# Performance work log

Hardware: AMD Instinct MI355X
Metric: run time of the kernel (lower is better)

The kernel has to match this reference:

```python
import jax, jax.numpy as jnp
import numpy as np

B, ENC, DEC, H, OUT = 4096, 168, 24, 64, 1
IN = 1 + 5 + 3 + 4 + 7  # 20


def _lstm_step(xt, h, c, Wih, Whh, bih, bhh):
    # PyTorch gate order: i, f, g, o
    g = xt @ Wih.T + h @ Whh.T + bih + bhh
    i, f, gg, o = jnp.split(g, 4, axis=-1)
    c = jax.nn.sigmoid(f) * c + jax.nn.sigmoid(i) * jnp.tanh(gg)
    h = jax.nn.sigmoid(o) * jnp.tanh(c)
    return h, c


def _lstm_layer(x, Wih, Whh, bih, bhh):
    # x: [T, B, in] -> ys: [T, B, H], final (h, c)
    h0 = jnp.zeros((x.shape[1], Whh.shape[1]), x.dtype)

    def step(carry, xt):
        h, c = _lstm_step(xt, carry[0], carry[1], Wih, Whh, bih, bhh)
        return (h, c), h

    (h, c), ys = jax.lax.scan(step, (h0, h0), x)
    return ys, h, c


def setup_inputs() -> dict:
    key = jax.random.key(0)
    ks = jax.random.split(key, 24)
    rn = lambda k, s, sc=0.05: jax.random.normal(k, s, jnp.float32) * sc
    inp = {
        "input_p_q": rn(ks[0], (B, ENC, 1), 1.0),
        "input_time": jax.random.randint(ks[1], (B, ENC, 4), 0, 8),
        "label_p": rn(ks[2], (B, ENC), 1.0),
        "decoder_time": jax.random.randint(ks[3], (B, DEC, 4), 0, 8),
        # encoder LSTM layer 0
        "enc0_Wih": rn(ks[4], (4 * H, IN)), "enc0_Whh": rn(ks[5], (4 * H, H)),
        "enc0_bih": rn(ks[6], (4 * H,)), "enc0_bhh": rn(ks[7], (4 * H,)),
        # encoder LSTM layer 1
        "enc1_Wih": rn(ks[8], (4 * H, H)), "enc1_Whh": rn(ks[9], (4 * H, H)),
        "enc1_bih": rn(ks[10], (4 * H,)), "enc1_bhh": rn(ks[11], (4 * H,)),
        # decoder LSTMCell (input = OUT + 19 = 20)
        "dec_Wih": rn(ks[12], (4 * H, OUT + 19)), "dec_Whh": rn(ks[13], (4 * H, H)),
        "dec_bih": rn(ks[14], (4 * H,)), "dec_bhh": rn(ks[15], (4 * H,)),
        # output projection
        "Wout": rn(ks[16], (OUT, H)), "bout": rn(ks[17], (OUT,)),
        # embeddings
        "emb_hour": rn(ks[18], (24, 5)), "emb_wd": rn(ks[19], (8, 3)),
        "emb_mo": rn(ks[20], (13, 4)), "emb_woy": rn(ks[21], (54, 7)),
    }
    return inp


def reference(input_p_q, input_time, label_p, decoder_time,
              enc0_Wih, enc0_Whh, enc0_bih, enc0_bhh,
              enc1_Wih, enc1_Whh, enc1_bih, enc1_bhh,
              dec_Wih, dec_Whh, dec_bih, dec_bhh,
              Wout, bout, emb_hour, emb_wd, emb_mo, emb_woy):
    def time_feats(t):  # t: [B, T, 4] int -> [B, T, 19]
        return jnp.concatenate([emb_hour[t[:, :, 0]], emb_wd[t[:, :, 1]],
                                emb_mo[t[:, :, 2]], emb_woy[t[:, :, 3]]], axis=-1)

    input_q = label_p[:, :ENC, None]                      # [B, ENC, 1]
    enc_in = jnp.concatenate([input_q, time_feats(input_time)], axis=-1)  # [B, ENC, 20]
    x = enc_in.transpose(1, 0, 2)                         # [ENC, B, 20]
    ys0, _, _ = _lstm_layer(x, enc0_Wih, enc0_Whh, enc0_bih, enc0_bhh)
    _, h1, c1 = _lstm_layer(ys0, enc1_Wih, enc1_Whh, enc1_bih, enc1_bhh)

    dec_feat = time_feats(decoder_time).transpose(1, 0, 2)  # [DEC, B, 19]
    prev0 = label_p[:, ENC - 1, None]                       # [B, 1]

    def dec_step(carry, ft):
        h, c, prev = carry
        xin = jnp.concatenate([prev, ft], axis=-1)          # [B, 20]
        h, c = _lstm_step(xin, h, c, dec_Wih, dec_Whh, dec_bih, dec_bhh)
        out = h @ Wout.T + bout                             # [B, OUT]
        return (h, c, out), out

    _, outs = jax.lax.scan(dec_step, (h1, c1, prev0), dec_feat)
    return outs.transpose(1, 0, 2)                          # [B, DEC, OUT]
```

## Files before the change

### kernel.cpp

```cpp
#include <hip/hip_runtime.h>

#define DEVFN __device__ __forceinline__

typedef float  f32x4  __attribute__((ext_vector_type(4)));
typedef short  bf16x8 __attribute__((ext_vector_type(8)));

constexpr int ENC = 168;
constexpr int DEC = 24;
constexpr int BT  = 16;
constexpr int NBLK = 4096 / BT;

constexpr float LOG2E  = 1.4426950408889634f;
constexpr float LOG2E2 = 2.8853900817779268f;

constexpr int W0F = 0;
constexpr int W1F = 24576;
constexpr int WDF = 57344;
constexpr int F_B0   = 40960;
constexpr int F_B1   = 41216;
constexpr int F_BD   = 41472;
constexpr int F_WOUT = 41728;
constexpr int F_BOUT = 41792;
constexpr int F_EMB  = 41793;
constexpr int NEMB = 574;

DEVFN ushort f2bf(float v) {
    unsigned b = __float_as_uint(v);
    return (ushort)((b + 0x7FFFu + ((b >> 16) & 1u)) >> 16);
}
DEVFN float bf2f(ushort u) { return __uint_as_float(((unsigned)u) << 16); }
DEVFN unsigned cvt_pk_bf16(float a, float b) {
    unsigned r;
    asm("v_cvt_pk_bf16_f32 %0, %1, %2" : "=v"(r) : "v"(a), "v"(b));
    return r;
}
DEVFN float exp2n(float x) {
    float r;
    asm("v_exp_f32 %0, -%1" : "=v"(r) : "v"(x));
    return r;
}
DEVFN void pinv(bf16x8& v) { asm volatile("" : "+v"(v)); }
DEVFN void pinf(f32x4& v)  { asm volatile("" : "+v"(v)); }

DEVFN float lstm_cell(float gi, float gf, float gg, float go, float& c) {
    float a  = exp2n(fmaxf(gi, -21.f));
    float b  = exp2n(fmaxf(gg, -43.f));
    float f  = exp2n(gf);
    float sf = __builtin_amdgcn_rcpf(1.f + f);
    float it = (1.f - b) * __builtin_amdgcn_rcpf(fmaf(a, b, a + b + 1.f));
    c = fmaf(sf, c, it);
    float d  = exp2n(fmaxf(c, -15.f) * LOG2E2);
    float o  = exp2n(fmaxf(go, -21.f));
    return (1.f - d) * __builtin_amdgcn_rcpf(fmaf(o, d, o + d + 1.f));
}

__global__ void prep_kernel(
    const float* __restrict__ w0ih, const float* __restrict__ w0hh,
    const float* __restrict__ b0ih, const float* __restrict__ b0hh,
    const float* __restrict__ w1ih, const float* __restrict__ w1hh,
    const float* __restrict__ b1ih, const float* __restrict__ b1hh,
    const float* __restrict__ wdih, const float* __restrict__ wdhh,
    const float* __restrict__ bdih, const float* __restrict__ bdhh,
    const float* __restrict__ wout, const float* __restrict__ boutp,
    const float* __restrict__ eh,   const float* __restrict__ ewd,
    const float* __restrict__ emo,  const float* __restrict__ ewoy,
    void* __restrict__ ws)
{
    ushort* wsu = (ushort*)ws;
    float*  wsf = (float*)ws;
    const int total = 81920 + 1407;
    for (int idx = blockIdx.x * blockDim.x + threadIdx.x; idx < total;
         idx += gridDim.x * blockDim.x) {
        if (idx < 81920) {
            int layer, q;
            if (idx < W1F)      { layer = 0; q = idx; }
            else if (idx < WDF) { layer = 1; q = idx - W1F; }
            else                { layer = 2; q = idx - WDF; }
            int c  = q >> 13;
            int tt = (q >> 9) & 15;
            int l  = (q >> 3) & 63;
            int j  = q & 7;
            int k  = c * 32 + (l >> 4) * 8 + j;
            int n  = tt * 16 + (l & 15);
            float v = 0.f;
            if (layer == 0) {
                if (k < 20) v = w0ih[n * 20 + k];
                else if (k == 20) v = w0ih[n * 20];
                else if (k >= 32 && k < 96) v = w0hh[n * 64 + (k - 32)];
            } else if (layer == 1) {
                if (k < 64) v = w1ih[n * 64 + k];
                else        v = w1hh[n * 64 + (k - 64)];
            } else {
                if (k < 20) v = wdih[n * 20 + k];
                else if (k == 20) v = wdih[n * 20];
                else if (k >= 32 && k < 96) v = wdhh[n * 64 + (k - 32)];
            }
            v *= ((n >> 6) == 2) ? LOG2E2 : LOG2E;
            wsu[idx] = f2bf(v);
        } else {
            int f = idx - 81920;
            float v;
            if (f < 768) {
                float sc = (((f & 255) >> 6) == 2) ? LOG2E2 : LOG2E;
                if (f < 256)      v = (b0ih[f] + b0hh[f]) * sc;
                else if (f < 512) v = (b1ih[f - 256] + b1hh[f - 256]) * sc;
                else              v = (bdih[f - 512] + bdhh[f - 512]) * sc;
            }
            else if (f < 832) v = wout[f - 768];
            else if (f == 832) v = boutp[0];
            else {
                int e = f - 833;
                if (e < 120)      v = eh[e];
                else if (e < 144) v = ewd[e - 120];
                else if (e < 196) v = emo[e - 144];
                else              v = ewoy[e - 196];
            }
            wsf[40960 + f] = v;
        }
    }
}

DEVFN int offX(int k, int m) {
    return (m + 16 * (k >> 3)) * 8 + (k & 7);
}
DEVFN void store_h4(ushort* A, int off, const float* h) {
    unsigned h01 = cvt_pk_bf16(h[0], h[1]);
    unsigned h23 = cvt_pk_bf16(h[2], h[3]);
    asm volatile("" : "+v"(h01), "+v"(h23));
    unsigned long long p = ((unsigned long long)h23 << 32) | h01;
    *(unsigned long long*)(A + off) = p;
}
DEVFN void store_prev(ushort* A, int m, float v) {
    ushort hi = f2bf(v);
    A[offX(0, m)]  = hi;
    A[offX(20, m)] = f2bf(v - bf2f(hi));
}

__global__ __launch_bounds__(512)
__attribute__((amdgpu_waves_per_eu(2, 2)))
void lstm_mfma(
    const int* __restrict__ input_time, const float* __restrict__ label_p,
    const int* __restrict__ decoder_time, const void* __restrict__ ws,
    float* __restrict__ out)
{
    const ushort* wsu = (const ushort*)ws;
    const float*  wsf = (const float*)ws;

    __shared__ __align__(16) ushort Abuf[2][5 * 512];
    __shared__ float s_emb[NEMB];
    __shared__ float s_wout[64];
    __shared__ float sh1[16 * 68];
    __shared__ float s_bout;

    const int tid = threadIdx.x;
    const int w   = tid >> 6;
    const int l   = tid & 63;
    const int q   = l >> 4;
    const int m   = l & 15;
    const int wl  = w & 3;
    const bool isL0 = (w < 4);
    const int b0g = blockIdx.x * BT;
    const int u0  = wl * 16 + q * 4;

    const int hoff = (1 + (u0 >> 5)) * 512 +
                     (m + 16 * ((u0 & 31) >> 3)) * 8 + (u0 & 7) +
                     (isL0 ? 0 : 1024);

    for (int i = tid; i < 2 * 5 * 512; i += 512) ((ushort*)Abuf)[i] = 0;
    for (int i = tid; i < NEMB; i += 512) s_emb[i] = wsf[F_EMB + i];
    if (tid < 64) s_wout[tid] = wsf[F_WOUT + tid];
    if (tid == 0) s_bout = wsf[F_BOUT];

    bf16x8 wA[4][4];
    if (isL0) {
#pragma unroll
        for (int c = 0; c < 3; c++)
#pragma unroll
            for (int g = 0; g < 4; g++)
                wA[c][g] = *(const bf16x8*)(wsu + W0F +
                    (c * 16 + g * 4 + wl) * 512 + l * 8);
        wA[3][0] = wA[3][1] = wA[3][2] = wA[3][3] = bf16x8{0,0,0,0,0,0,0,0};
    } else {
#pragma unroll
        for (int c = 0; c < 4; c++)
#pragma unroll
            for (int g = 0; g < 4; g++)
                wA[c][g] = *(const bf16x8*)(wsu + W1F +
                    (c * 16 + g * 4 + wl) * 512 + l * 8);
    }
#pragma unroll
    for (int c = 0; c < 4; c++)
#pragma unroll
        for (int g = 0; g < 4; g++) pinv(wA[c][g]);

    f32x4 biasv[4];
#pragma unroll
    for (int g = 0; g < 4; g++) {
        biasv[g] = *(const f32x4*)(wsf + (isL0 ? F_B0 : F_B1) + g * 64 + u0);
        pinf(biasv[g]);
    }

    float cst[4] = {0.f, 0.f, 0.f, 0.f};

    const int kk1 = tid >> 4;
    const int kk2 = kk1 + 16;
    const bool bx2 = (tid < 64);
    int sel1 = 0, estr1 = 0, ebase1 = 0;
    if (kk1 >= 1) {
        int f = kk1 - 1;
        if (f < 5)       { sel1 = 0; estr1 = 5; ebase1 = 0   + f; }
        else if (f < 8)  { sel1 = 1; estr1 = 3; ebase1 = 120 + (f - 5); }
        else if (f < 12) { sel1 = 2; estr1 = 4; ebase1 = 144 + (f - 8); }
        else             { sel1 = 3; estr1 = 7; ebase1 = 196 + (f - 12); }
    }
    const int ebase2 = 196 + (kk2 - 13);

    __syncthreads();
    if (isL0) {
        if (kk1 == 0) {
            store_prev(Abuf[0], m, label_p[(b0g + m) * ENC]);
        } else {
            int idx = input_time[((b0g + m) * ENC) * 4 + sel1];
            Abuf[0][offX(kk1, m)] = f2bf(s_emb[ebase1 + idx * estr1]);
        }
        if (bx2) {
            int idx2 = input_time[((b0g + m) * ENC) * 4 + 3];
            Abuf[0][offX(kk2, m)] = f2bf(s_emb[ebase2 + idx2 * 7]);
        }
    }
    __syncthreads();

    for (int i = 0; i <= ENC; ++i) {
        const ushort* Ar = Abuf[i & 1];
        ushort* Aw = Abuf[(i + 1) & 1];
        const bool active = isL0 ? (i < ENC) : (i >= 1);

        float pre_f = 0.f; int pre_i1 = 0, pre_i2 = 0;
        const bool encX  = (i + 1 < ENC) && isL0;
        const bool decX0 = (i == ENC) && isL0;
        if (encX) {
            if (kk1 == 0) pre_f  = label_p[(b0g + m) * ENC + (i + 1)];
            else          pre_i1 = input_time[((b0g + m) * ENC + (i + 1)) * 4 + sel1];
            if (bx2)      pre_i2 = input_time[((b0g + m) * ENC + (i + 1)) * 4 + 3];
        } else if (decX0) {
            if (kk1 == 0) pre_f  = label_p[(b0g + m) * ENC + (ENC - 1)];
            else          pre_i1 = decoder_time[((b0g + m) * DEC) * 4 + sel1];
            if (bx2)      pre_i2 = decoder_time[((b0g + m) * DEC) * 4 + 3];
        }

        if (active) {
            f32x4 acc[4];
            if (isL0) {
                bf16x8 ah[3];
#pragma unroll
                for (int c = 0; c < 3; c++)
                    ah[c] = *(const bf16x8*)(Ar + c * 512 + l * 8);
#pragma unroll
                for (int g = 0; g < 4; g++)
                    acc[g] = __builtin_amdgcn_mfma_f32_16x16x32_bf16(
                        wA[0][g], ah[0], biasv[g], 0, 0, 0);
#pragma unroll
                for (int c = 1; c < 3; c++)
#pragma unroll
                    for (int g = 0; g < 4; g++)
                        acc[g] = __builtin_amdgcn_mfma_f32_16x16x32_bf16(
                            wA[c][g], ah[c], acc[g], 0, 0, 0);
            } else {
                bf16x8 ah[4];
#pragma unroll
                for (int c = 0; c < 4; c++)
                    ah[c] = *(const bf16x8*)(Ar + (1 + c) * 512 + l * 8);
#pragma unroll
                for (int g = 0; g < 4; g++)
                    acc[g] = __builtin_amdgcn_mfma_f32_16x16x32_bf16(
                        wA[0][g], ah[0], biasv[g], 0, 0, 0);
#pragma unroll
                for (int c = 1; c < 4; c++)
#pragma unroll
                    for (int g = 0; g < 4; g++)
                        acc[g] = __builtin_amdgcn_mfma_f32_16x16x32_bf16(
                            wA[c][g], ah[c], acc[g], 0, 0, 0);
            }
            float hv[4];
#pragma unroll
            for (int r = 0; r < 4; r++)
                hv[r] = lstm_cell(acc[0][r], acc[1][r], acc[2][r], acc[3][r], cst[r]);
            store_h4(Aw, hoff, hv);
        }
        if (encX || decX0) {
            if (kk1 == 0) store_prev(Aw, m, pre_f);
            else          Aw[offX(kk1, m)] = f2bf(s_emb[ebase1 + pre_i1 * estr1]);
            if (bx2)      Aw[offX(kk2, m)] = f2bf(s_emb[ebase2 + pre_i2 * 7]);
        }
        __syncthreads();
    }

    if (!isL0) {
#pragma unroll
        for (int c = 0; c < 3; c++)
#pragma unroll
            for (int g = 0; g < 4; g++)
                wA[c][g] = *(const bf16x8*)(wsu + WDF +
                    (c * 16 + g * 4 + wl) * 512 + l * 8);
#pragma unroll
        for (int c = 0; c < 3; c++)
#pragma unroll
            for (int g = 0; g < 4; g++) pinv(wA[c][g]);
#pragma unroll
        for (int g = 0; g < 4; g++) {
            biasv[g] = *(const f32x4*)(wsf + F_BD + g * 64 + u0);
            pinf(biasv[g]);
        }
    }

    for (int t = 0; t < DEC; ++t) {
        const ushort* Ar = Abuf[(t + 1) & 1];
        ushort* Aw = Abuf[t & 1];

        int pre_i1 = 0, pre_i2 = 0;
        const bool dX = (t + 1 < DEC) && isL0;
        if (dX) {
            if (kk1 >= 1) pre_i1 = decoder_time[((b0g + m) * DEC + (t + 1)) * 4 + sel1];
            if (bx2)      pre_i2 = decoder_time[((b0g + m) * DEC + (t + 1)) * 4 + 3];
        }

        if (!isL0) {
            bf16x8 ah[3];
            ah[0] = *(const bf16x8*)(Ar + 0 * 512 + l * 8);
            ah[1] = *(const bf16x8*)(Ar + 3 * 512 + l * 8);
            ah[2] = *(const bf16x8*)(Ar + 4 * 512 + l * 8);
            f32x4 acc[4];
#pragma unroll
            for (int g = 0; g < 4; g++)
                acc[g] = __builtin_amdgcn_mfma_f32_16x16x32_bf16(
                    wA[0][g], ah[0], biasv[g], 0, 0, 0);
#pragma unroll
            for (int c = 1; c < 3; c++)
#pragma unroll
                for (int g = 0; g < 4; g++)
                    acc[g] = __builtin_amdgcn_mfma_f32_16x16x32_bf16(
                        wA[c][g], ah[c], acc[g], 0, 0, 0);
            float hv[4];
#pragma unroll
            for (int r = 0; r < 4; r++)
                hv[r] = lstm_cell(acc[0][r], acc[1][r], acc[2][r], acc[3][r], cst[r]);
            store_h4(Aw, hoff, hv);
            *(f32x4*)&sh1[m * 68 + u0] = *(f32x4*)hv;
        }
        if (dX && kk1 >= 1) Aw[offX(kk1, m)] = f2bf(s_emb[ebase1 + pre_i1 * estr1]);
        if (dX && bx2)      Aw[offX(kk2, m)] = f2bf(s_emb[ebase2 + pre_i2 * 7]);
        __syncthreads();

        if (tid < 16) {
            float a = s_bout;
#pragma unroll 16
            for (int u = 0; u < 64; u++) a = fmaf(s_wout[u], sh1[tid * 68 + u], a);
            out[(b0g + tid) * DEC + t] = a;
            if (t + 1 < DEC) store_prev(Aw, tid, a);
        }
        __syncthreads();
    }
}

extern "C" void kernel_launch(void* const* d_in, const int* in_sizes, int n_in,
                              void* d_out, int out_size, void* d_ws, size_t ws_size,
                              hipStream_t stream)
{
    typedef const float* fp;
    const int* input_time   = (const int*)d_in[1];
    fp         label_p      = (fp)d_in[2];
    const int* decoder_time = (const int*)d_in[3];

    prep_kernel<<<128, 256, 0, stream>>>(
        (fp)d_in[4],  (fp)d_in[5],  (fp)d_in[6],  (fp)d_in[7],
        (fp)d_in[8],  (fp)d_in[9],  (fp)d_in[10], (fp)d_in[11],
        (fp)d_in[12], (fp)d_in[13], (fp)d_in[14], (fp)d_in[15],
        (fp)d_in[16], (fp)d_in[17],
        (fp)d_in[18], (fp)d_in[19], (fp)d_in[20], (fp)d_in[21],
        d_ws);

    lstm_mfma<<<NBLK, 512, 0, stream>>>(
        input_time, label_p, decoder_time, d_ws, (float*)d_out);
}
```

Before: 285.2 us.

## Merge both encoder layers into each wave with 256-thread blocks

Each block drops from 8 waves (4 for layer 0, 4 for layer 1) to 4 waves, and every wave now computes both the layer-0 and the layer-1 gate MFMAs plus both cell updates for its hidden-unit slice. Both layers' weights are kept in registers, and waves_per_eu is set to 1. The goal is to cut the per-step barrier cost and wave imbalance by doubling the independent MFMA work per wave, which gives more ILP within a step. The cost is higher register pressure, fewer resident waves per CU, and twice the serial work per wave on each timestep.

Result: slower. 360.8 us (+26.5%).

```diff
diff --git a/kernel.cpp b/kernel.cpp
--- a/kernel.cpp
+++ b/kernel.cpp
@@ -136,8 +136,8 @@
     A[offX(20, m)] = f2bf(v - bf2f(hi));
 }
 
-__global__ __launch_bounds__(512)
-__attribute__((amdgpu_waves_per_eu(2, 2)))
+__global__ __launch_bounds__(256)
+__attribute__((amdgpu_waves_per_eu(1, 1)))
 void lstm_mfma(
     const int* __restrict__ input_time, const float* __restrict__ label_p,
     const int* __restrict__ decoder_time, const void* __restrict__ ws,
@@ -157,50 +157,45 @@
     const int l   = tid & 63;
     const int q   = l >> 4;
     const int m   = l & 15;
-    const int wl  = w & 3;
-    const bool isL0 = (w < 4);
     const int b0g = blockIdx.x * BT;
-    const int u0  = wl * 16 + q * 4;
-
-    const int hoff = (1 + (u0 >> 5)) * 512 +
-                     (m + 16 * ((u0 & 31) >> 3)) * 8 + (u0 & 7) +
-                     (isL0 ? 0 : 1024);
-
-    for (int i = tid; i < 2 * 5 * 512; i += 512) ((ushort*)Abuf)[i] = 0;
-    for (int i = tid; i < NEMB; i += 512) s_emb[i] = wsf[F_EMB + i];
+    const int u0  = w * 16 + q * 4;
+
+    const int hoff0 = (1 + (u0 >> 5)) * 512 +
+                      (m + 16 * ((u0 & 31) >> 3)) * 8 + (u0 & 7);
+    const int hoff1 = hoff0 + 1024;
+
+    for (int i = tid; i < 2 * 5 * 512; i += 256) ((ushort*)Abuf)[i] = 0;
+    for (int i = tid; i < NEMB; i += 256) s_emb[i] = wsf[F_EMB + i];
     if (tid < 64) s_wout[tid] = wsf[F_WOUT + tid];
     if (tid == 0) s_bout = wsf[F_BOUT];
 
-    bf16x8 wA[4][4];
-    if (isL0) {
-#pragma unroll
-        for (int c = 0; c < 3; c++)
-#pragma unroll
-            for (int g = 0; g < 4; g++)
-                wA[c][g] = *(const bf16x8*)(wsu + W0F +
-                    (c * 16 + g * 4 + wl) * 512 + l * 8);
-        wA[3][0] = wA[3][1] = wA[3][2] = wA[3][3] = bf16x8{0,0,0,0,0,0,0,0};
-    } else {
-#pragma unroll
-        for (int c = 0; c < 4; c++)
-#pragma unroll
-            for (int g = 0; g < 4; g++)
-                wA[c][g] = *(const bf16x8*)(wsu + W1F +
-                    (c * 16 + g * 4 + wl) * 512 + l * 8);
-    }
+    bf16x8 wA0[3][4], wA1[4][4];
+#pragma unroll
+    for (int c = 0; c < 3; c++)
+#pragma unroll
+        for (int g = 0; g < 4; g++) {
+            wA0[c][g] = *(const bf16x8*)(wsu + W0F +
+                (c * 16 + g * 4 + w) * 512 + l * 8);
+            pinv(wA0[c][g]);
+        }
 #pragma unroll
     for (int c = 0; c < 4; c++)
 #pragma unroll
-        for (int g = 0; g < 4; g++) pinv(wA[c][g]);
-
-    f32x4 biasv[4];
+        for (int g = 0; g < 4; g++) {
+            wA1[c][g] = *(const bf16x8*)(wsu + W1F +
+                (c * 16 + g * 4 + w) * 512 + l * 8);
+            pinv(wA1[c][g]);
+        }
+    f32x4 bias0[4], bias1[4];
 #pragma unroll
     for (int g = 0; g < 4; g++) {
-        biasv[g] = *(const f32x4*)(wsf + (isL0 ? F_B0 : F_B1) + g * 64 + u0);
-        pinf(biasv[g]);
-    }
-
-    float cst[4] = {0.f, 0.f, 0.f, 0.f};
+        bias0[g] = *(const f32x4*)(wsf + F_B0 + g * 64 + u0);
+        bias1[g] = *(const f32x4*)(wsf + F_B1 + g * 64 + u0);
+        pinf(bias0[g]); pinf(bias1[g]);
+    }
+
+    float cst0[4] = {0.f, 0.f, 0.f, 0.f};
+    float cst1[4] = {0.f, 0.f, 0.f, 0.f};
 
     const int kk1 = tid >> 4;
     const int kk2 = kk1 + 16;
@@ -216,7 +211,7 @@
     const int ebase2 = 196 + (kk2 - 13);
 
     __syncthreads();
-    if (isL0) {
+    {
         if (kk1 == 0) {
             store_prev(Abuf[0], m, label_p[(b0g + m) * ENC]);
         } else {
@@ -233,11 +228,11 @@
     for (int i = 0; i <= ENC; ++i) {
         const ushort* Ar = Abuf[i & 1];
         ushort* Aw = Abuf[(i + 1) & 1];
-        const bool active = isL0 ? (i < ENC) : (i >= 1);
+        const bool L0 = (i < ENC), L1 = (i >= 1);
 
         float pre_f = 0.f; int pre_i1 = 0, pre_i2 = 0;
-        const bool encX  = (i + 1 < ENC) && isL0;
-        const bool decX0 = (i == ENC) && isL0;
+        const bool encX  = (i + 1 < ENC);
+        const bool decX0 = (i == ENC);
         if (encX) {
             if (kk1 == 0) pre_f  = label_p[(b0g + m) * ENC + (i + 1)];
             else          pre_i1 = input_time[((b0g + m) * ENC + (i + 1)) * 4 + sel1];
@@ -248,44 +243,49 @@
             if (bx2)      pre_i2 = decoder_time[((b0g + m) * DEC) * 4 + 3];
         }
 
-        if (active) {
-            f32x4 acc[4];
-            if (isL0) {
-                bf16x8 ah[3];
-#pragma unroll
-                for (int c = 0; c < 3; c++)
-                    ah[c] = *(const bf16x8*)(Ar + c * 512 + l * 8);
+        bf16x8 a[5];
+#pragma unroll
+        for (int c = 0; c < 5; c++)
+            a[c] = *(const bf16x8*)(Ar + c * 512 + l * 8);
+
+        f32x4 acc0[4], acc1[4];
+        if (L0) {
+#pragma unroll
+            for (int g = 0; g < 4; g++)
+                acc0[g] = __builtin_amdgcn_mfma_f32_16x16x32_bf16(
+                    wA0[0][g], a[0], bias0[g], 0, 0, 0);
+#pragma unroll
+            for (int c = 1; c < 3; c++)
 #pragma unroll
                 for (int g = 0; g < 4; g++)
-                    acc[g] = __builtin_amdgcn_mfma_f32_16x16x32_bf16(
-                        wA[0][g], ah[0], biasv[g], 0, 0, 0);
-#pragma unroll
-                for (int c = 1; c < 3; c++)
-#pragma unroll
-                    for (int g = 0; g < 4; g++)
-                        acc[g] = __builtin_amdgcn_mfma_f32_16x16x32_bf16(
-                            wA[c][g], ah[c], acc[g], 0, 0, 0);
-            } else {
-                bf16x8 ah[4];
-#pragma unroll
-                for (int c = 0; c < 4; c++)
-                    ah[c] = *(const bf16x8*)(Ar + (1 + c) * 512 + l * 8);
+                    acc0[g] = __builtin_amdgcn_mfma_f32_16x16x32_bf16(
+                        wA0[c][g], a[c], acc0[g], 0, 0, 0);
+        }
+        if (L1) {
+#pragma unroll
+            for (int g = 0; g < 4; g++)
+                acc1[g] = __builtin_amdgcn_mfma_f32_16x16x32_bf16(
+                    wA1[0][g], a[1], bias1[g], 0, 0, 0);
+#pragma unroll
+            for (int c = 1; c < 4; c++)
 #pragma unroll
                 for (int g = 0; g < 4; g++)
-                    acc[g] = __builtin_amdgcn_mfma_f32_16x16x32_bf16(
-                        wA[0][g], ah[0], biasv[g], 0, 0, 0);
-#pragma unroll
-                for (int c = 1; c < 4; c++)
-#pragma unroll
-                    for (int g = 0; g < 4; g++)
-                        acc[g] = __builtin_amdgcn_mfma_f32_16x16x32_bf16(
-                            wA[c][g], ah[c], acc[g], 0, 0, 0);
-            }
+                    acc1[g] = __builtin_amdgcn_mfma_f32_16x16x32_bf16(
+                        wA1[c][g], a[1 + c], acc1[g], 0, 0, 0);
+        }
+        if (L0) {
             float hv[4];
 #pragma unroll
             for (int r = 0; r < 4; r++)
-                hv[r] = lstm_cell(acc[0][r], acc[1][r], acc[2][r], acc[3][r], cst[r]);
-            store_h4(Aw, hoff, hv);
+                hv[r] = lstm_cell(acc0[0][r], acc0[1][r], acc0[2][r], acc0[3][r], cst0[r]);
+            store_h4(Aw, hoff0, hv);
+        }
+        if (L1) {
+            float hv[4];
+#pragma unroll
+            for (int r = 0; r < 4; r++)
+                hv[r] = lstm_cell(acc1[0][r], acc1[1][r], acc1[2][r], acc1[3][r], cst1[r]);
+            store_h4(Aw, hoff1, hv);
         }
         if (encX || decX0) {
             if (kk1 == 0) store_prev(Aw, m, pre_f);
@@ -295,22 +295,18 @@
         __syncthreads();
     }
 
-    if (!isL0) {
-#pragma unroll
-        for (int c = 0; c < 3; c++)
-#pragma unroll
-            for (int g = 0; g < 4; g++)
-                wA[c][g] = *(const bf16x8*)(wsu + WDF +
-                    (c * 16 + g * 4 + wl) * 512 + l * 8);
-#pragma unroll
-        for (int c = 0; c < 3; c++)
-#pragma unroll
-            for (int g = 0; g < 4; g++) pinv(wA[c][g]);
+#pragma unroll
+    for (int c = 0; c < 3; c++)
 #pragma unroll
         for (int g = 0; g < 4; g++) {
-            biasv[g] = *(const f32x4*)(wsf + F_BD + g * 64 + u0);
-            pinf(biasv[g]);
-        }
+            wA0[c][g] = *(const bf16x8*)(wsu + WDF +
+                (c * 16 + g * 4 + w) * 512 + l * 8);
+            pinv(wA0[c][g]);
+        }
+#pragma unroll
+    for (int g = 0; g < 4; g++) {
+        bias0[g] = *(const f32x4*)(wsf + F_BD + g * 64 + u0);
+        pinf(bias0[g]);
     }
 
     for (int t = 0; t < DEC; ++t) {
@@ -318,13 +314,13 @@
         ushort* Aw = Abuf[t & 1];
 
         int pre_i1 = 0, pre_i2 = 0;
-        const bool dX = (t + 1 < DEC) && isL0;
+        const bool dX = (t + 1 < DEC);
         if (dX) {
             if (kk1 >= 1) pre_i1 = decoder_time[((b0g + m) * DEC + (t + 1)) * 4 + sel1];
             if (bx2)      pre_i2 = decoder_time[((b0g + m) * DEC + (t + 1)) * 4 + 3];
         }
 
-        if (!isL0) {
+        {
             bf16x8 ah[3];
             ah[0] = *(const bf16x8*)(Ar + 0 * 512 + l * 8);
             ah[1] = *(const bf16x8*)(Ar + 3 * 512 + l * 8);
@@ -333,18 +329,18 @@
 #pragma unroll
             for (int g = 0; g < 4; g++)
                 acc[g] = __builtin_amdgcn_mfma_f32_16x16x32_bf16(
-                    wA[0][g], ah[0], biasv[g], 0, 0, 0);
+                    wA0[0][g], ah[0], bias0[g], 0, 0, 0);
 #pragma unroll
             for (int c = 1; c < 3; c++)
 #pragma unroll
                 for (int g = 0; g < 4; g++)
                     acc[g] = __builtin_amdgcn_mfma_f32_16x16x32_bf16(
-                        wA[c][g], ah[c], acc[g], 0, 0, 0);
+                        wA0[c][g], ah[c], acc[g], 0, 0, 0);
             float hv[4];
 #pragma unroll
             for (int r = 0; r < 4; r++)
-                hv[r] = lstm_cell(acc[0][r], acc[1][r], acc[2][r], acc[3][r], cst[r]);
-            store_h4(Aw, hoff, hv);
+                hv[r] = lstm_cell(acc[0][r], acc[1][r], acc[2][r], acc[3][r], cst1[r]);
+            store_h4(Aw, hoff1, hv);
             *(f32x4*)&sh1[m * 68 + u0] = *(f32x4*)hv;
         }
         if (dX && kk1 >= 1) Aw[offX(kk1, m)] = f2bf(s_emb[ebase1 + pre_i1 * estr1]);
@@ -379,6 +375,6 @@
         (fp)d_in[18], (fp)d_in[19], (fp)d_in[20], (fp)d_in[21],
         d_ws);
 
-    lstm_mfma<<<NBLK, 512, 0, stream>>>(
+    lstm_mfma<<<NBLK, 256, 0, stream>>>(
         input_time, label_p, decoder_time, d_ws, (float*)d_out);
 }
```
